# Kernel tuning notes

Hardware: AMD Instinct MI355X
Metric: run time of the kernel (lower is better)

## Reference

```python
import jax, jax.numpy as jnp
import numpy as np

NDIM = (256, 256, 256)
NMIN = (-1.0, -1.0, -1.0)
NMAX = (1.0, 1.0, 1.0)
NDELTA = tuple((NMAX[i] - NMIN[i]) / (NDIM[i] - 1.0) for i in range(3))
MIN_DEG, MAX_DEG = 0, 10
ANNEALED_ALPHA = 1.0
EPS = 1e-12


def compute_grad(grid):
    # central differences on the voxel grid with edge padding -> [N, 3]
    g = grid.reshape(NDIM[0], NDIM[1], NDIM[2])
    p = jnp.pad(g, ((1, 1), (1, 1), (1, 1)), mode='edge')
    dx = (p[2:, 1:-1, 1:-1] - p[:-2, 1:-1, 1:-1]) / (2.0 * NDELTA[0])
    dy = (p[1:-1, 2:, 1:-1] - p[1:-1, :-2, 1:-1]) / (2.0 * NDELTA[1])
    dz = (p[1:-1, 1:-1, 2:] - p[1:-1, 1:-1, :-2]) / (2.0 * NDELTA[2])
    return jnp.stack([dx, dy, dz], axis=-1).reshape(-1, 3)


def trilinear3(data, pts):
    # data: [N, 4] flattened voxel features, pts: [B, 3] -> [B, 4]
    x = (pts[..., 0] - NMIN[0]) / NDELTA[0]
    y = (pts[..., 1] - NMIN[1]) / NDELTA[1]
    z = (pts[..., 2] - NMIN[2]) / NDELTA[2]
    x0f = jnp.floor(x); y0f = jnp.floor(y); z0f = jnp.floor(z)
    xd = (x - x0f)[..., None]
    yd = (y - y0f)[..., None]
    zd = (z - z0f)[..., None]
    x0 = jnp.clip(x0f.astype(jnp.int32), 0, NDIM[0] - 1)
    x1 = jnp.clip(x0f.astype(jnp.int32) + 1, 0, NDIM[0] - 1)
    y0 = jnp.clip(y0f.astype(jnp.int32), 0, NDIM[1] - 1)
    y1 = jnp.clip(y0f.astype(jnp.int32) + 1, 0, NDIM[1] - 1)
    z0 = jnp.clip(z0f.astype(jnp.int32), 0, NDIM[2] - 1)
    z1 = jnp.clip(z0f.astype(jnp.int32) + 1, 0, NDIM[2] - 1)
    sYZ, sZ = NDIM[1] * NDIM[2], NDIM[2]
    gat = lambda i, j, k: data[sYZ * i + sZ * j + k]
    c00 = gat(x0, y0, z0) * (1 - xd) + gat(x1, y0, z0) * xd
    c01 = gat(x0, y0, z1) * (1 - xd) + gat(x1, y0, z1) * xd
    c10 = gat(x0, y1, z0) * (1 - xd) + gat(x1, y1, z0) * xd
    c11 = gat(x0, y1, z1) * (1 - xd) + gat(x1, y1, z1) * xd
    c0 = c00 * (1 - yd) + c10 * yd
    c1 = c01 * (1 - yd) + c11 * yd
    return c0 * (1 - zd) + c1 * zd


def annealed_pos_enc(x, alpha):
    # nerfies-style windowed positional encoding with identity concat
    bands = jnp.arange(MIN_DEG, MAX_DEG, dtype=x.dtype)  # [D]
    scales = 2.0 ** bands
    xb = x[..., None, :] * scales[:, None]               # [..., D, 3]
    four = jnp.sin(jnp.stack([xb, xb + 0.5 * jnp.pi], axis=-2))  # [..., D, 2, 3]
    w = jnp.clip(alpha - bands, 0.0, 1.0)
    w = 0.5 * (1.0 - jnp.cos(jnp.pi * w))                # cosine easing window
    four = four * w[:, None, None]
    four = four.reshape(x.shape[:-1] + (-1,))            # [..., D*6]
    return jnp.concatenate([x, four], axis=-1)           # [..., 3 + D*6]


def mlp(feats, w0, b0, w1, b1, w2, b2, w3, b3, wo, bo):
    # net_depth=4, skip_layer=2 -> concat inputs after layer index 2
    h = jax.nn.relu(feats @ w0 + b0)
    h = jax.nn.relu(h @ w1 + b1)
    h = jax.nn.relu(h @ w2 + b2)
    h = jnp.concatenate([h, feats], axis=-1)
    h = jax.nn.relu(h @ w3 + b3)
    return h @ wo + bo


def safe_l2_norm(v):
    return jnp.sqrt(jnp.sum(v * v, axis=-1, keepdims=True) + EPS)


def setup_inputs() -> dict:
    key = jax.random.key(0)
    ks = jax.random.split(key, 8)
    B = 1048576
    N = NDIM[0] * NDIM[1] * NDIM[2]
    x = jax.random.uniform(ks[0], (B, 3), jnp.float32, -1.0, 1.0)
    grid = jax.random.normal(ks[1], (N, 1), jnp.float32)
    glorot = lambda k, fi, fo: jax.random.normal(k, (fi, fo), jnp.float32) * jnp.sqrt(2.0 / (fi + fo))
    return {
        'x': x, 'grid': grid,
        'w0': glorot(ks[2], 63, 128), 'b0': jnp.zeros((128,), jnp.float32),
        'w1': glorot(ks[3], 128, 128), 'b1': jnp.zeros((128,), jnp.float32),
        'w2': glorot(ks[4], 128, 128), 'b2': jnp.zeros((128,), jnp.float32),
        'w3': glorot(ks[5], 191, 128), 'b3': jnp.zeros((128,), jnp.float32),
        'wo': jax.random.normal(ks[6], (128, 3), jnp.float32) * 1e-5,  # output_init normal(1e-5)
        'bo': jnp.zeros((3,), jnp.float32),
    }


def reference(x, grid, w0, b0, w1, b1, w2, b2, w3, b3, wo, bo):
    data = jnp.concatenate([grid, compute_grad(grid)], axis=-1)  # [N, 4]
    ret = trilinear3(data, x)                                    # [B, 4]
    feats = annealed_pos_enc(x[:, None], ANNEALED_ALPHA * MAX_DEG)  # [B, 1, 63]
    raw = mlp(feats, w0, b0, w1, b1, w2, b2, w3, b3, wo, bo)[:, 0]  # [B, 3]
    # residual + direct output: rotate gradient vector by axis-angle raw
    theta = safe_l2_norm(raw)
    e = raw / theta
    cond = ret[..., 1:]
    a = safe_l2_norm(cond)
    v = cond / a
    rot = a * (jnp.cos(theta) * v + jnp.sin(theta) * jnp.cross(e, v)
               + (1.0 - jnp.cos(theta)) * jnp.sum(e * v, axis=-1, keepdims=True) * e)
    return (ret[..., :1], ret[..., 1:], rot)
```

## Files before the change

### kernel.cpp

```cpp
#include <hip/hip_runtime.h>


typedef __attribute__((ext_vector_type(8))) short bf8;
typedef __attribute__((ext_vector_type(4))) float f4;

__device__ __forceinline__ float bf2f(unsigned int u) {
    union { float f; unsigned int i; } v; v.i = u << 16; return v.f;
}
__device__ __forceinline__ unsigned short f2bf(float f) {
    union { float f; unsigned int i; } v; v.f = f;
    unsigned int x = v.i;
    return (unsigned short)((x + 0x7fffu + ((x >> 16) & 1u)) >> 16);
}
__device__ __forceinline__ float gv(const float* __restrict__ g, int i, int j, int k) {
    return g[(i * 256 + j) * 256 + k];
}

#define WS_TOTAL 67584
#define DG_OFF_SH 131072
#define WS_NEED (262144ull + 16777216ull * 8ull)

__global__ __launch_bounds__(256) void swizzle_w(
    const float* __restrict__ w0, const float* __restrict__ w1,
    const float* __restrict__ w2, const float* __restrict__ w3,
    const float* __restrict__ wo, unsigned short* __restrict__ ws)
{
    int idx = blockIdx.x * 256 + threadIdx.x;
    if (idx >= WS_TOTAL) return;
    const float* src; int base, NT, Kact, Nact, ld;
    if (idx < 8192)       { src = w0; base = 0;     NT = 8; Kact = 63;  Nact = 128; ld = 128; }
    else if (idx < 24576) { src = w1; base = 8192;  NT = 8; Kact = 128; Nact = 128; ld = 128; }
    else if (idx < 40960) { src = w2; base = 24576; NT = 8; Kact = 128; Nact = 128; ld = 128; }
    else if (idx < 65536) { src = w3; base = 40960; NT = 8; Kact = 191; Nact = 128; ld = 128; }
    else                  { src = wo; base = 65536; NT = 1; Kact = 128; Nact = 3;   ld = 3;   }
    int local = idx - base;
    int j = local & 7;
    int lane = (local >> 3) & 63;
    int chunk = local >> 9;
    int nt = chunk % NT, kt = chunk / NT;
    int k = kt * 32 + ((lane >> 4) << 3) + j;
    int n = nt * 16 + (lane & 15);
    float v = (k < Kact && n < Nact) ? src[k * ld + n] : 0.0f;
    ws[idx] = f2bf(v);
}

__global__ __launch_bounds__(256) void make_dgrid(
    const float* __restrict__ g, unsigned short* __restrict__ dg)
{
    const int t  = blockIdx.x * 256 + threadIdx.x;
    const int k0 = (t & 63) << 2;
    const int j  = (t >> 6) & 255;
    const int i  = t >> 14;
    const float* row = g + (i * 256 + j) * 256;
    const f4 self = *(const f4*)(row + k0);
    const f4 xp = *(const f4*)(g + (min(i + 1, 255) * 256 + j) * 256 + k0);
    const f4 xm = *(const f4*)(g + (max(i - 1, 0)   * 256 + j) * 256 + k0);
    const f4 yp = *(const f4*)(g + (i * 256 + min(j + 1, 255)) * 256 + k0);
    const f4 ym = *(const f4*)(g + (i * 256 + max(j - 1, 0))   * 256 + k0);
    const float zlo = row[max(k0 - 1, 0)];
    const float zhi = row[min(k0 + 4, 255)];
    float zv[6] = {zlo, self[0], self[1], self[2], self[3], zhi};
    unsigned short o[16];
    #pragma unroll
    for (int q = 0; q < 4; ++q) {
        o[q * 4 + 0] = f2bf(self[q]);
        o[q * 4 + 1] = f2bf((xp[q] - xm[q]) * 63.75f);
        o[q * 4 + 2] = f2bf((yp[q] - ym[q]) * 63.75f);
        o[q * 4 + 3] = f2bf((zv[q + 2] - zv[q]) * 63.75f);
    }
    unsigned short* dst = dg + (size_t)(((i * 256 + j) * 256 + k0)) * 4;
    *(uint4*)(dst)     = *(const uint4*)(o);
    *(uint4*)(dst + 8) = *(const uint4*)(o + 8);
}

#define WV_SH 6656
#define HSTRIDE 136
#define FSTRIDE 72

template<bool FAST>
__global__ __launch_bounds__(256, 3) void voxmlp(
    const float* __restrict__ x, const float* __restrict__ grid,
    const unsigned short* __restrict__ ws, const unsigned short* __restrict__ dg,
    const float* __restrict__ b0, const float* __restrict__ b1,
    const float* __restrict__ b2, const float* __restrict__ b3,
    const float* __restrict__ bo,
    float* __restrict__ out, int B)
{
    __shared__ unsigned short smem[WV_SH * 4];

    const int lane = threadIdx.x & 63;
    const int wave = threadIdx.x >> 6;
    const int quad = lane >> 4;
    const int lm   = lane & 15;
    unsigned short* bufH = smem + wave * WV_SH;
    unsigned short* fbuf = bufH + 32 * HSTRIDE;

    const int pbase = blockIdx.x * 128 + wave * 32;

    const int p2   = lane & 31;
    const int role = lane >> 5;
    const int pid  = pbase + p2;

    const float px = x[pid * 3 + 0];
    const float py = x[pid * 3 + 1];
    const float pz = x[pid * 3 + 2];

    if (role == 0) {
        const float fx = (px + 1.0f) * 127.5f;
        const float fy = (py + 1.0f) * 127.5f;
        const float fz = (pz + 1.0f) * 127.5f;
        const float fx0 = floorf(fx), fy0 = floorf(fy), fz0 = floorf(fz);
        const float xd = fx - fx0, yd = fy - fy0, zd = fz - fz0;
        const int ix0 = min(max((int)fx0, 0), 255);
        const int iy0 = min(max((int)fy0, 0), 255);
        const int iz0 = min(max((int)fz0, 0), 255);
        const int ix1 = min(ix0 + 1, 255);
        const int iy1 = min(iy0 + 1, 255);
        const int iz1 = min(iz0 + 1, 255);

        float ret0 = 0.f, c1 = 0.f, c2 = 0.f, c3 = 0.f;
        if (FAST) {
            #pragma unroll
            for (int c = 0; c < 8; ++c) {
                const int i = (c & 4) ? ix1 : ix0;
                const int j = (c & 2) ? iy1 : iy0;
                const int k = (c & 1) ? iz1 : iz0;
                const float wgt = ((c & 4) ? xd : 1.0f - xd) *
                                  ((c & 2) ? yd : 1.0f - yd) *
                                  ((c & 1) ? zd : 1.0f - zd);
                const uint2 w = *(const uint2*)(dg + (size_t)((i * 256 + j) * 256 + k) * 4);
                ret0 = fmaf(wgt, bf2f(w.x & 0xffffu), ret0);
                c1   = fmaf(wgt, bf2f(w.x >> 16),     c1);
                c2   = fmaf(wgt, bf2f(w.y & 0xffffu), c2);
                c3   = fmaf(wgt, bf2f(w.y >> 16),     c3);
            }
        } else {
            #pragma unroll
            for (int c = 0; c < 8; ++c) {
                const int i = (c & 4) ? ix1 : ix0;
                const int j = (c & 2) ? iy1 : iy0;
                const int k = (c & 1) ? iz1 : iz0;
                const float wgt = ((c & 4) ? xd : 1.0f - xd) *
                                  ((c & 2) ? yd : 1.0f - yd) *
                                  ((c & 1) ? zd : 1.0f - zd);
                const float v  = gv(grid, i, j, k);
                const float gx = (gv(grid, min(i + 1, 255), j, k) - gv(grid, max(i - 1, 0), j, k)) * 63.75f;
                const float gy = (gv(grid, i, min(j + 1, 255), k) - gv(grid, i, max(j - 1, 0), k)) * 63.75f;
                const float gz = (gv(grid, i, j, min(k + 1, 255)) - gv(grid, i, j, max(k - 1, 0))) * 63.75f;
                ret0 = fmaf(wgt, v,  ret0);
                c1   = fmaf(wgt, gx, c1);
                c2   = fmaf(wgt, gy, c2);
                c3   = fmaf(wgt, gz, c3);
            }
        }
        out[pid] = ret0;
        out[B + pid * 3 + 0] = c1;
        out[B + pid * 3 + 1] = c2;
        out[B + pid * 3 + 2] = c3;
        float* cst = (float*)(fbuf + p2 * FSTRIDE + 64);
        cst[0] = c1; cst[1] = c2; cst[2] = c3;
    } else {
        unsigned short* fb = fbuf + p2 * FSTRIDE;
        fb[0] = f2bf(px); fb[1] = f2bf(py); fb[2] = f2bf(pz);
        fb[63] = 0;
        float s = 1.0f;
        #pragma unroll
        for (int b = 0; b < 10; ++b) {
            const int base = 3 + b * 6;
            float sv, cv;
            __sincosf(px * s, &sv, &cv); fb[base + 0] = f2bf(sv); fb[base + 3] = f2bf(cv);
            __sincosf(py * s, &sv, &cv); fb[base + 1] = f2bf(sv); fb[base + 4] = f2bf(cv);
            __sincosf(pz * s, &sv, &cv); fb[base + 2] = f2bf(sv); fb[base + 5] = f2bf(cv);
            s *= 2.0f;
        }
    }
    __builtin_amdgcn_s_barrier();

    bf8 af[2][6];
    const int arow0 = lm * HSTRIDE + quad * 8;
    const int frow0 = lm * FSTRIDE + quad * 8;

    auto store_tile = [&](f4 acc, int pt, int ut) {
        unsigned int lo = (unsigned int)f2bf(fmaxf(acc[0], 0.f))
                        | ((unsigned int)f2bf(fmaxf(acc[1], 0.f)) << 16);
        unsigned int hi = (unsigned int)f2bf(fmaxf(acc[2], 0.f))
                        | ((unsigned int)f2bf(fmaxf(acc[3], 0.f)) << 16);
        uint2 pk; pk.x = lo; pk.y = hi;
        *(uint2*)(bufH + (pt * 16 + lm) * HSTRIDE + ut * 16 + quad * 4) = pk;
    };

    #pragma unroll
    for (int pt = 0; pt < 2; ++pt)
        #pragma unroll
        for (int kt = 0; kt < 2; ++kt)
            af[pt][kt] = *(const bf8*)(fbuf + pt * 16 * FSTRIDE + frow0 + kt * 32);
    #pragma unroll
    for (int ut = 0; ut < 8; ++ut) {
        bf8 wf[2];
        #pragma unroll
        for (int kt = 0; kt < 2; ++kt)
            wf[kt] = *(const bf8*)(ws + 0 + (((kt * 8 + ut) * 64 + lane) << 3));
        const f4 bias = *(const f4*)(b0 + ut * 16 + quad * 4);
        #pragma unroll
        for (int pt = 0; pt < 2; ++pt) {
            f4 acc = bias;
            #pragma unroll
            for (int kt = 0; kt < 2; ++kt)
                acc = __builtin_amdgcn_mfma_f32_16x16x32_bf16(wf[kt], af[pt][kt], acc, 0, 0, 0);
            store_tile(acc, pt, ut);
        }
    }
    __builtin_amdgcn_s_barrier();

    #pragma unroll
    for (int layer = 0; layer < 2; ++layer) {
        const unsigned short* wsl = ws + (layer == 0 ? 8192 : 24576);
        const float* bias_p = (layer == 0) ? b1 : b2;
        #pragma unroll
        for (int pt = 0; pt < 2; ++pt)
            #pragma unroll
            for (int kt = 0; kt < 4; ++kt)
                af[pt][kt] = *(const bf8*)(bufH + pt * 16 * HSTRIDE + arow0 + kt * 32);
        #pragma unroll
        for (int ut = 0; ut < 8; ++ut) {
            bf8 wf[4];
            #pragma unroll
            for (int kt = 0; kt < 4; ++kt)
                wf[kt] = *(const bf8*)(wsl + (((kt * 8 + ut) * 64 + lane) << 3));
            const f4 bias = *(const f4*)(bias_p + ut * 16 + quad * 4);
            #pragma unroll
            for (int pt = 0; pt < 2; ++pt) {
                f4 acc = bias;
                #pragma unroll
                for (int kt = 0; kt < 4; ++kt)
                    acc = __builtin_amdgcn_mfma_f32_16x16x32_bf16(wf[kt], af[pt][kt], acc, 0, 0, 0);
                store_tile(acc, pt, ut);
            }
        }
        __builtin_amdgcn_s_barrier();
    }

    #pragma unroll
    for (int pt = 0; pt < 2; ++pt) {
        #pragma unroll
        for (int kt = 0; kt < 4; ++kt)
            af[pt][kt] = *(const bf8*)(bufH + pt * 16 * HSTRIDE + arow0 + kt * 32);
        #pragma unroll
        for (int kk = 0; kk < 2; ++kk)
            af[pt][4 + kk] = *(const bf8*)(fbuf + pt * 16 * FSTRIDE + frow0 + kk * 32);
    }
    #pragma unroll
    for (int ut = 0; ut < 8; ++ut) {
        bf8 wf[6];
        #pragma unroll
        for (int kt = 0; kt < 6; ++kt)
            wf[kt] = *(const bf8*)(ws + 40960 + (((kt * 8 + ut) * 64 + lane) << 3));
        const f4 bias = *(const f4*)(b3 + ut * 16 + quad * 4);
        #pragma unroll
        for (int pt = 0; pt < 2; ++pt) {
            f4 acc = bias;
            #pragma unroll
            for (int kt = 0; kt < 6; ++kt)
                acc = __builtin_amdgcn_mfma_f32_16x16x32_bf16(wf[kt], af[pt][kt], acc, 0, 0, 0);
            store_tile(acc, pt, ut);
        }
    }
    __builtin_amdgcn_s_barrier();

    #pragma unroll
    for (int pt = 0; pt < 2; ++pt)
        #pragma unroll
        for (int kt = 0; kt < 4; ++kt)
            af[pt][kt] = *(const bf8*)(bufH + pt * 16 * HSTRIDE + arow0 + kt * 32);
    bf8 wf[4];
    #pragma unroll
    for (int kt = 0; kt < 4; ++kt)
        wf[kt] = *(const bf8*)(ws + 65536 + ((kt * 64 + lane) << 3));

    #pragma unroll
    for (int pt = 0; pt < 2; ++pt) {
        f4 acc;
        #pragma unroll
        for (int r = 0; r < 4; ++r) {
            const int u = quad * 4 + r;
            acc[r] = (u < 3) ? bo[u] : 0.0f;
        }
        #pragma unroll
        for (int kt = 0; kt < 4; ++kt)
            acc = __builtin_amdgcn_mfma_f32_16x16x32_bf16(wf[kt], af[pt][kt], acc, 0, 0, 0);

        const int pp = pt * 16 + lm;
        const float* cst = (const float*)(fbuf + pp * FSTRIDE + 64);
        const float g1 = cst[0], g2 = cst[1], g3 = cst[2];
        const float r0 = acc[0], r1 = acc[1], r2 = acc[2];
        const float theta = sqrtf(fmaf(r0, r0, fmaf(r1, r1, r2 * r2)) + 1e-12f);
        const float e0 = r0 / theta, e1 = r1 / theta, e2 = r2 / theta;
        const float a = sqrtf(fmaf(g1, g1, fmaf(g2, g2, g3 * g3)) + 1e-12f);
        const float v0 = g1 / a, v1 = g2 / a, v2 = g3 / a;
        const float ct = cosf(theta), st = sinf(theta);
        const float cx = e1 * v2 - e2 * v1;
        const float cy = e2 * v0 - e0 * v2;
        const float cz = e0 * v1 - e1 * v0;
        const float om = (1.0f - ct) * (e0 * v0 + e1 * v1 + e2 * v2);
        if (quad == 0) {
            const int pid2 = pbase + pp;
            out[4 * B + pid2 * 3 + 0] = a * (ct * v0 + st * cx + om * e0);
            out[4 * B + pid2 * 3 + 1] = a * (ct * v1 + st * cy + om * e1);
            out[4 * B + pid2 * 3 + 2] = a * (ct * v2 + st * cz + om * e2);
        }
    }
}

extern "C" void kernel_launch(void* const* d_in, const int* in_sizes, int n_in,
                              void* d_out, int out_size, void* d_ws, size_t ws_size,
                              hipStream_t stream)
{
    const float* x    = (const float*)d_in[0];
    const float* grid = (const float*)d_in[1];
    const float* w0   = (const float*)d_in[2];
    const float* b0   = (const float*)d_in[3];
    const float* w1   = (const float*)d_in[4];
    const float* b1   = (const float*)d_in[5];
    const float* w2   = (const float*)d_in[6];
    const float* b2   = (const float*)d_in[7];
    const float* w3   = (const float*)d_in[8];
    const float* b3   = (const float*)d_in[9];
    const float* wo   = (const float*)d_in[10];
    const float* bo   = (const float*)d_in[11];
    float* out = (float*)d_out;
    unsigned short* ws = (unsigned short*)d_ws;
    unsigned short* dg = ws + DG_OFF_SH;

    const int B = in_sizes[0] / 3;
    swizzle_w<<<(WS_TOTAL + 255) / 256, 256, 0, stream>>>(w0, w1, w2, w3, wo, ws);
    if (ws_size >= WS_NEED) {
        make_dgrid<<<16384, 256, 0, stream>>>(grid, dg);
        voxmlp<true><<<B / 128, 256, 0, stream>>>(x, grid, ws, dg, b0, b1, b2, b3, bo, out, B);
    } else {
        voxmlp<false><<<B / 128, 256, 0, stream>>>(x, grid, ws, dg, b0, b1, b2, b3, bo, out, B);
    }
}
```

Baseline: 387.1 us.

## Merge prep kernels, pack bf16 conversions, permute PE features, use fast rcp/sincos

Merges the weight swizzle and gradient-grid build into one prep launch, which removes a kernel launch and lets the two jobs overlap. Replaces the software bf16 rounding with the hardware packed convert instruction in the gradient grid build, the positional encoding and the hidden-layer stores. Reorders the positional-encoding features so sin/cos pairs are packed and written as vector stores, and permutes the w0/w3 rows to match. Swaps divisions for reciprocals and cosf/sinf for __sincosf in the rotation epilogue, which trades some accuracy for speed.

```diff
diff --git a/kernel.cpp b/kernel.cpp
--- a/kernel.cpp
+++ b/kernel.cpp
@@ -12,65 +12,85 @@
     unsigned int x = v.i;
     return (unsigned short)((x + 0x7fffu + ((x >> 16) & 1u)) >> 16);
 }
+__device__ __forceinline__ unsigned int pkbf(float a, float b) {
+    unsigned int r;
+    asm("v_cvt_pk_bf16_f32 %0, %1, %2" : "=v"(r) : "v"(a), "v"(b));
+    return r;
+}
 __device__ __forceinline__ float gv(const float* __restrict__ g, int i, int j, int k) {
     return g[(i * 256 + j) * 256 + k];
 }
+__device__ __forceinline__ int featmap(int kp) {
+    if (kp < 3) return kp;
+    if (kp == 3) return -1;
+    const int m = kp - 4, b = m / 6, r = m - 6 * b, d = r >> 1, c = r & 1;
+    return 3 + 6 * b + 3 * c + d;
+}
 
 #define WS_TOTAL 67584
+#define SWZ_BLOCKS 264
 #define DG_OFF_SH 131072
 #define WS_NEED (262144ull + 16777216ull * 8ull)
 
-__global__ __launch_bounds__(256) void swizzle_w(
+__global__ __launch_bounds__(256) void prep(
+    const float* __restrict__ g,
     const float* __restrict__ w0, const float* __restrict__ w1,
     const float* __restrict__ w2, const float* __restrict__ w3,
-    const float* __restrict__ wo, unsigned short* __restrict__ ws)
+    const float* __restrict__ wo,
+    unsigned short* __restrict__ ws, unsigned short* __restrict__ dg,
+    int do_dgrid)
 {
-    int idx = blockIdx.x * 256 + threadIdx.x;
-    if (idx >= WS_TOTAL) return;
-    const float* src; int base, NT, Kact, Nact, ld;
-    if (idx < 8192)       { src = w0; base = 0;     NT = 8; Kact = 63;  Nact = 128; ld = 128; }
-    else if (idx < 24576) { src = w1; base = 8192;  NT = 8; Kact = 128; Nact = 128; ld = 128; }
-    else if (idx < 40960) { src = w2; base = 24576; NT = 8; Kact = 128; Nact = 128; ld = 128; }
-    else if (idx < 65536) { src = w3; base = 40960; NT = 8; Kact = 191; Nact = 128; ld = 128; }
-    else                  { src = wo; base = 65536; NT = 1; Kact = 128; Nact = 3;   ld = 3;   }
-    int local = idx - base;
-    int j = local & 7;
-    int lane = (local >> 3) & 63;
-    int chunk = local >> 9;
-    int nt = chunk % NT, kt = chunk / NT;
-    int k = kt * 32 + ((lane >> 4) << 3) + j;
-    int n = nt * 16 + (lane & 15);
-    float v = (k < Kact && n < Nact) ? src[k * ld + n] : 0.0f;
-    ws[idx] = f2bf(v);
-}
-
-__global__ __launch_bounds__(256) void make_dgrid(
-    const float* __restrict__ g, unsigned short* __restrict__ dg)
-{
-    const int t  = blockIdx.x * 256 + threadIdx.x;
-    const int k0 = (t & 63) << 2;
-    const int j  = (t >> 6) & 255;
-    const int i  = t >> 14;
-    const float* row = g + (i * 256 + j) * 256;
-    const f4 self = *(const f4*)(row + k0);
-    const f4 xp = *(const f4*)(g + (min(i + 1, 255) * 256 + j) * 256 + k0);
-    const f4 xm = *(const f4*)(g + (max(i - 1, 0)   * 256 + j) * 256 + k0);
-    const f4 yp = *(const f4*)(g + (i * 256 + min(j + 1, 255)) * 256 + k0);
-    const f4 ym = *(const f4*)(g + (i * 256 + max(j - 1, 0))   * 256 + k0);
-    const float zlo = row[max(k0 - 1, 0)];
-    const float zhi = row[min(k0 + 4, 255)];
-    float zv[6] = {zlo, self[0], self[1], self[2], self[3], zhi};
-    unsigned short o[16];
-    #pragma unroll
-    for (int q = 0; q < 4; ++q) {
-        o[q * 4 + 0] = f2bf(self[q]);
-        o[q * 4 + 1] = f2bf((xp[q] - xm[q]) * 63.75f);
-        o[q * 4 + 2] = f2bf((yp[q] - ym[q]) * 63.75f);
-        o[q * 4 + 3] = f2bf((zv[q + 2] - zv[q]) * 63.75f);
-    }
-    unsigned short* dst = dg + (size_t)(((i * 256 + j) * 256 + k0)) * 4;
-    *(uint4*)(dst)     = *(const uint4*)(o);
-    *(uint4*)(dst + 8) = *(const uint4*)(o + 8);
+    const int bid = blockIdx.x;
+    if (bid < SWZ_BLOCKS) {
+        int idx = bid * 256 + threadIdx.x;
+        const float* src; int base, NT, Kact, Nact, ld;
+        if (idx < 8192)       { src = w0; base = 0;     NT = 8; Kact = 64;  Nact = 128; ld = 128; }
+        else if (idx < 24576) { src = w1; base = 8192;  NT = 8; Kact = 128; Nact = 128; ld = 128; }
+        else if (idx < 40960) { src = w2; base = 24576; NT = 8; Kact = 128; Nact = 128; ld = 128; }
+        else if (idx < 65536) { src = w3; base = 40960; NT = 8; Kact = 192; Nact = 128; ld = 128; }
+        else                  { src = wo; base = 65536; NT = 1; Kact = 128; Nact = 3;   ld = 3;   }
+        int local = idx - base;
+        int j = local & 7;
+        int lane = (local >> 3) & 63;
+        int chunk = local >> 9;
+        int nt = chunk % NT, kt = chunk / NT;
+        int k = kt * 32 + ((lane >> 4) << 3) + j;
+        int n = nt * 16 + (lane & 15);
+        float v = 0.0f;
+        if (k < Kact && n < Nact) {
+            int ko = k;
+            if (base == 0)            ko = featmap(k);
+            else if (base == 40960 && k >= 128) {
+                int f = featmap(k - 128);
+                ko = (f < 0) ? -1 : 128 + f;
+            }
+            if (ko >= 0) v = src[ko * ld + n];
+        }
+        ws[idx] = f2bf(v);
+    } else if (do_dgrid) {
+        const int t  = (bid - SWZ_BLOCKS) * 256 + threadIdx.x;
+        const int k0 = (t & 63) << 2;
+        const int j  = (t >> 6) & 255;
+        const int i  = t >> 14;
+        const float* row = g + (i * 256 + j) * 256;
+        const f4 self = *(const f4*)(row + k0);
+        const f4 xp = *(const f4*)(g + (min(i + 1, 255) * 256 + j) * 256 + k0);
+        const f4 xm = *(const f4*)(g + (max(i - 1, 0)   * 256 + j) * 256 + k0);
+        const f4 yp = *(const f4*)(g + (i * 256 + min(j + 1, 255)) * 256 + k0);
+        const f4 ym = *(const f4*)(g + (i * 256 + max(j - 1, 0))   * 256 + k0);
+        const float zlo = row[max(k0 - 1, 0)];
+        const float zhi = row[min(k0 + 4, 255)];
+        float zv[6] = {zlo, self[0], self[1], self[2], self[3], zhi};
+        unsigned int o[8];
+        #pragma unroll
+        for (int q = 0; q < 4; ++q) {
+            o[q * 2 + 0] = pkbf(self[q], (xp[q] - xm[q]) * 63.75f);
+            o[q * 2 + 1] = pkbf((yp[q] - ym[q]) * 63.75f, (zv[q + 2] - zv[q]) * 63.75f);
+        }
+        unsigned short* dst = dg + (size_t)(((i * 256 + j) * 256 + k0)) * 4;
+        *(uint4*)(dst)     = *(const uint4*)(o);
+        *(uint4*)(dst + 8) = *(const uint4*)(o + 4);
+    }
 }
 
 #define WV_SH 6656
@@ -160,19 +180,25 @@
         float* cst = (float*)(fbuf + p2 * FSTRIDE + 64);
         cst[0] = c1; cst[1] = c2; cst[2] = c3;
     } else {
+        unsigned int f[32];
+        f[0] = pkbf(px, py);
+        f[1] = pkbf(pz, 0.0f);
+        const float crd[3] = {px, py, pz};
+        float s = 1.0f;
+        #pragma unroll
+        for (int b = 0; b < 10; ++b) {
+            #pragma unroll
+            for (int d = 0; d < 3; ++d) {
+                float sv, cv;
+                __sincosf(crd[d] * s, &sv, &cv);
+                f[2 + b * 3 + d] = pkbf(sv, cv);
+            }
+            s *= 2.0f;
+        }
         unsigned short* fb = fbuf + p2 * FSTRIDE;
-        fb[0] = f2bf(px); fb[1] = f2bf(py); fb[2] = f2bf(pz);
-        fb[63] = 0;
-        float s = 1.0f;
-        #pragma unroll
-        for (int b = 0; b < 10; ++b) {
-            const int base = 3 + b * 6;
-            float sv, cv;
-            __sincosf(px * s, &sv, &cv); fb[base + 0] = f2bf(sv); fb[base + 3] = f2bf(cv);
-            __sincosf(py * s, &sv, &cv); fb[base + 1] = f2bf(sv); fb[base + 4] = f2bf(cv);
-            __sincosf(pz * s, &sv, &cv); fb[base + 2] = f2bf(sv); fb[base + 5] = f2bf(cv);
-            s *= 2.0f;
-        }
+        #pragma unroll
+        for (int i = 0; i < 8; ++i)
+            *(uint4*)(fb + i * 8) = *(const uint4*)(&f[i * 4]);
     }
     __builtin_amdgcn_s_barrier();
 
@@ -181,11 +207,9 @@
     const int frow0 = lm * FSTRIDE + quad * 8;
 
     auto store_tile = [&](f4 acc, int pt, int ut) {
-        unsigned int lo = (unsigned int)f2bf(fmaxf(acc[0], 0.f))
-                        | ((unsigned int)f2bf(fmaxf(acc[1], 0.f)) << 16);
-        unsigned int hi = (unsigned int)f2bf(fmaxf(acc[2], 0.f))
-                        | ((unsigned int)f2bf(fmaxf(acc[3], 0.f)) << 16);
-        uint2 pk; pk.x = lo; pk.y = hi;
+        uint2 pk;
+        pk.x = pkbf(fmaxf(acc[0], 0.f), fmaxf(acc[1], 0.f));
+        pk.y = pkbf(fmaxf(acc[2], 0.f), fmaxf(acc[3], 0.f));
         *(uint2*)(bufH + (pt * 16 + lm) * HSTRIDE + ut * 16 + quad * 4) = pk;
     };
 
@@ -294,10 +318,13 @@
         const float g1 = cst[0], g2 = cst[1], g3 = cst[2];
         const float r0 = acc[0], r1 = acc[1], r2 = acc[2];
         const float theta = sqrtf(fmaf(r0, r0, fmaf(r1, r1, r2 * r2)) + 1e-12f);
-        const float e0 = r0 / theta, e1 = r1 / theta, e2 = r2 / theta;
+        const float it = __builtin_amdgcn_rcpf(theta);
+        const float e0 = r0 * it, e1 = r1 * it, e2 = r2 * it;
         const float a = sqrtf(fmaf(g1, g1, fmaf(g2, g2, g3 * g3)) + 1e-12f);
-        const float v0 = g1 / a, v1 = g2 / a, v2 = g3 / a;
-        const float ct = cosf(theta), st = sinf(theta);
+        const float ia = __builtin_amdgcn_rcpf(a);
+        const float v0 = g1 * ia, v1 = g2 * ia, v2 = g3 * ia;
+        float st, ct;
+        __sincosf(theta, &st, &ct);
         const float cx = e1 * v2 - e2 * v1;
         const float cy = e2 * v0 - e0 * v2;
         const float cz = e0 * v1 - e1 * v0;
@@ -332,11 +359,11 @@
     unsigned short* dg = ws + DG_OFF_SH;
 
     const int B = in_sizes[0] / 3;
-    swizzle_w<<<(WS_TOTAL + 255) / 256, 256, 0, stream>>>(w0, w1, w2, w3, wo, ws);
-    if (ws_size >= WS_NEED) {
-        make_dgrid<<<16384, 256, 0, stream>>>(grid, dg);
+    const int fast = (ws_size >= WS_NEED) ? 1 : 0;
+    const int nprep = fast ? (SWZ_BLOCKS + 16384) : SWZ_BLOCKS;
+    prep<<<nprep, 256, 0, stream>>>(grid, w0, w1, w2, w3, wo, ws, dg, fast);
+    if (fast)
         voxmlp<true><<<B / 128, 256, 0, stream>>>(x, grid, ws, dg, b0, b1, b2, b3, bo, out, B);
-    } else {
+    else
         voxmlp<false><<<B / 128, 256, 0, stream>>>(x, grid, ws, dg, b0, b1, b2, b3, bo, out, B);
-    }
-}
+}
```

Result: faster. 372.2 us (-3.9%).
